# Optimization experiments

Hardware: AMD Instinct MI355X
Metric: run time of the kernel (lower is better)

Reference implementation:

```python
import jax, jax.numpy as jnp
import numpy as np

B, N, H, T = 256, 512, 2048, 64
DT = 0.05  # time spacing so tanh-MLP dynamics stay well-behaved


def setup_inputs() -> dict:
    key = jax.random.key(0)
    k0, k1, k2 = jax.random.split(key, 3)
    y_0 = jax.random.normal(k0, (B, N), dtype=jnp.float32)
    t_eval = jnp.arange(T, dtype=jnp.float32) * DT
    # dy/dt neural network: f(t, y) = tanh(y @ W1 + b1) @ W2 + b2
    W1 = jax.random.normal(k1, (N, H), dtype=jnp.float32) * 0.05
    b1 = jnp.zeros((H,), dtype=jnp.float32)
    W2 = jax.random.normal(k2, (H, N), dtype=jnp.float32) * 0.05
    b2 = jnp.zeros((N,), dtype=jnp.float32)
    return {"y_0": y_0, "t_eval": t_eval, "W1": W1, "b1": b1, "W2": W2, "b2": b2}


def reference(y_0, t_eval, W1, b1, W2, b2):
    """RK4 odeint: returns (y_t [B,T,N], t_t [T], y_loss [B]).

    One classical RK4 step per consecutive pair of t_eval points;
    continuous loss defaults to zero (matches _zero_loss).
    """
    def f(t, y):
        # time-invariant neural dynamics; t kept for signature fidelity
        return jnp.tanh(y @ W1 + b1) @ W2 + b2

    def rk4_step(y, ts):
        t0, t1 = ts[0], ts[1]
        h = t1 - t0
        k1 = f(t0, y)
        k2 = f(t0 + h * 0.5, y + (h * 0.5) * k1)
        k3 = f(t0 + h * 0.5, y + (h * 0.5) * k2)
        k4 = f(t1, y + h * k3)
        y_new = y + (h / 6.0) * (k1 + 2.0 * k2 + 2.0 * k3 + k4)
        return y_new, y_new

    ts_pairs = jnp.stack([t_eval[:-1], t_eval[1:]], axis=1)  # [T-1, 2]
    _, ys = jax.lax.scan(rk4_step, y_0, ts_pairs)            # [T-1, B, N]
    y_t = jnp.concatenate([y_0[None], ys], axis=0)           # [T, B, N]
    y_t = jnpp_transpose(y_t) if False else jnp.transpose(y_t, (1, 0, 2))  # [B, T, N]
    y_loss = jnp.zeros(y_0.shape[:-1], dtype=y_0.dtype)      # zero continuous loss
    return y_t, t_eval, y_loss
```

## Files before the change

kernel.cpp:

```cpp
#include <hip/hip_runtime.h>
#include <hip/hip_bf16.h>

#define Bsz 256
#define Nd  512
#define Hd  2048
#define Td  64
#define OFF_T (Bsz * Td * Nd)
#define OFF_L (OFF_T + Td)
#define LDU 514
#define LDZ 136

typedef __attribute__((ext_vector_type(8))) short short8;
typedef __attribute__((ext_vector_type(4))) float f32x4;

static __device__ __forceinline__ unsigned short f2bf(float x) {
  unsigned u = __builtin_bit_cast(unsigned, x);
  u += 0x7FFFu + ((u >> 16) & 1u);
  return (unsigned short)(u >> 16);
}
static __device__ __forceinline__ float fast_tanh(float x) {
  float ex = __expf(2.0f * x);
  return 1.0f - 2.0f / (ex + 1.0f);
}
static __device__ __forceinline__ unsigned long long lda64(const void* p) {
  return __hip_atomic_load((const unsigned long long*)p, __ATOMIC_RELAXED,
                           __HIP_MEMORY_SCOPE_AGENT);
}
static __device__ __forceinline__ void sta64(void* p, unsigned long long v) {
  __hip_atomic_store((unsigned long long*)p, v, __ATOMIC_RELAXED,
                     __HIP_MEMORY_SCOPE_AGENT);
}
static __device__ __forceinline__ unsigned lda32(const unsigned* p) {
  return __hip_atomic_load(p, __ATOMIC_RELAXED, __HIP_MEMORY_SCOPE_AGENT);
}
static __device__ __forceinline__ void sta32(unsigned* p, unsigned v) {
  __hip_atomic_store(p, v, __ATOMIC_RELAXED, __HIP_MEMORY_SCOPE_AGENT);
}

__launch_bounds__(256, 1)
__global__ void ode_df(const float* __restrict__ y0g, const float* __restrict__ te,
                       const float* __restrict__ W1, const float* __restrict__ b1,
                       const float* __restrict__ W2, const float* __restrict__ b2,
                       float* __restrict__ out, unsigned* __restrict__ flagZ,
                       unsigned* __restrict__ flagK,
                       float* __restrict__ kS, unsigned short* __restrict__ Zg) {
  __shared__ unsigned short Ulds[16 * LDU];
  __shared__ unsigned short Zlds[16 * LDZ];
  __shared__ float red[4][16][33];
  __shared__ char spad[56 * 1024];

  const int blk = blockIdx.x;
  const int g = blk & 15, il = blk >> 4;
  const int tid = threadIdx.x;
  const int wv = tid >> 6, lane = tid & 63;
  const int lr = lane & 15, lk = lane >> 4;

  if (te[0] == 1.0e30f) {
    ((volatile char*)spad)[tid] = (char)tid;
    out[0] = ((volatile char*)spad)[0];
  }

  short8 w1f[2][16];
  {
    const int hbase = il * 128 + wv * 32;
    #pragma unroll
    for (int n = 0; n < 2; ++n) {
      const int col = hbase + n * 16 + lr;
      #pragma unroll
      for (int kt = 0; kt < 16; ++kt) {
        short8 v;
        #pragma unroll
        for (int jj = 0; jj < 8; ++jj)
          v[jj] = (short)f2bf(W1[(kt * 32 + lk * 8 + jj) * Hd + col]);
        w1f[n][kt] = v;
      }
    }
  }
  short8 w2f[2][16];
  {
    #pragma unroll
    for (int n = 0; n < 2; ++n) {
      const int col = il * 32 + n * 16 + lr;
      #pragma unroll
      for (int kt = 0; kt < 16; ++kt) {
        short8 v;
        #pragma unroll
        for (int jj = 0; jj < 8; ++jj)
          v[jj] = (short)f2bf(W2[(wv * 512 + kt * 32 + lk * 8 + jj) * Nd + col]);
        w2f[n][kt] = v;
      }
    }
  }
  float b1c[2];
  b1c[0] = b1[il * 128 + wv * 32 + lr];
  b1c[1] = b1[il * 128 + wv * 32 + 16 + lr];

  const int r  = tid >> 4;
  const int cq = tid & 15;
  const int cb = cq * 32;
  const int rowg = g * 16 + r;
  const int c2 = (tid & 15) * 2;
  const int rowe = tid >> 4;
  const float b2e0 = b2[il * 32 + c2], b2e1 = b2[il * 32 + c2 + 1];

  float yv[32];
  #pragma unroll
  for (int gg = 0; gg < 8; ++gg) {
    f32x4 v = *(const f32x4*)&y0g[rowg * Nd + cb + gg * 4];
    yv[gg * 4 + 0] = v[0]; yv[gg * 4 + 1] = v[1];
    yv[gg * 4 + 2] = v[2]; yv[gg * 4 + 3] = v[3];
  }
  float acc_y[32];
  #pragma unroll
  for (int p = 0; p < 32; ++p) acc_y[p] = 0.0f;

  if (cq == il) {
    #pragma unroll
    for (int gg = 0; gg < 8; ++gg) {
      f32x4 v = {yv[gg * 4], yv[gg * 4 + 1], yv[gg * 4 + 2], yv[gg * 4 + 3]};
      *(f32x4*)&out[rowg * (Td * Nd) + cb + gg * 4] = v;
    }
  }
  if (blk == 0) {
    if (tid < Td) out[OFF_T + tid] = te[tid];
    out[OFF_L + tid] = 0.0f;
  }

  unsigned* flZ = flagZ + g * 16;
  unsigned* flK = flagK + g * 16;

  int j = 0;
  for (int t = 0; t < Td - 1; ++t) {
    const float h = te[t + 1] - te[t];
    for (int e = 1; e <= 4; ++e) {
      float kv[32];
      if (!(e == 1 && t == 0)) {
        const unsigned tgt = (unsigned)j;
        const unsigned* p = flK + (tid & 15);
        for (;;) {
          unsigned v = lda32(p);
          if (__all((int)(v >= tgt))) break;
          __builtin_amdgcn_s_sleep(1);
        }
        const float* kbase = &kS[rowg * Nd + cb];
        #pragma unroll
        for (int p2 = 0; p2 < 16; ++p2) {
          unsigned long long q = lda64(kbase + p2 * 2);
          kv[2 * p2 + 0] = __builtin_bit_cast(float, (unsigned)(q & 0xFFFFFFFFull));
          kv[2 * p2 + 1] = __builtin_bit_cast(float, (unsigned)(q >> 32));
        }
      }
      if (e == 1) {
        if (t > 0) {
          const float hp6 = (te[t] - te[t - 1]) * (1.0f / 6.0f);
          #pragma unroll
          for (int p2 = 0; p2 < 32; ++p2) yv[p2] += hp6 * (acc_y[p2] + kv[p2]);
          if (cq == il) {
            #pragma unroll
            for (int gg = 0; gg < 8; ++gg) {
              f32x4 v = {yv[gg * 4], yv[gg * 4 + 1], yv[gg * 4 + 2], yv[gg * 4 + 3]};
              *(f32x4*)&out[rowg * (Td * Nd) + t * Nd + cb + gg * 4] = v;
            }
          }
        }
        #pragma unroll
        for (int p2 = 0; p2 < 32; ++p2) acc_y[p2] = 0.0f;
        #pragma unroll
        for (int gg = 0; gg < 4; ++gg) {
          short8 s;
          #pragma unroll
          for (int p2 = 0; p2 < 8; ++p2) s[p2] = (short)f2bf(yv[gg * 8 + p2]);
          *(short8*)&Ulds[r * LDU + cb + gg * 8] = s;
        }
      } else {
        const float c = (e == 4) ? h : 0.5f * h;
        const float w = (e == 2) ? 1.0f : 2.0f;
        #pragma unroll
        for (int gg = 0; gg < 4; ++gg) {
          short8 s;
          #pragma unroll
          for (int p2 = 0; p2 < 8; ++p2) {
            const int idx = gg * 8 + p2;
            acc_y[idx] += w * kv[idx];
            s[p2] = (short)f2bf(yv[idx] + c * kv[idx]);
          }
          *(short8*)&Ulds[r * LDU + cb + gg * 8] = s;
        }
      }
      __syncthreads();

      f32x4 acc1_0 = {0.f, 0.f, 0.f, 0.f}, acc1_1 = {0.f, 0.f, 0.f, 0.f};
      {
        const int abase = lr * LDU + lk * 8;
        #pragma unroll
        for (int kt = 0; kt < 16; ++kt) {
          short8 a = *(const short8*)&Ulds[abase + kt * 32];
          acc1_0 = __builtin_amdgcn_mfma_f32_16x16x32_bf16(a, w1f[0][kt], acc1_0, 0, 0, 0);
          acc1_1 = __builtin_amdgcn_mfma_f32_16x16x32_bf16(a, w1f[1][kt], acc1_1, 0, 0, 0);
        }
      }
      #pragma unroll
      for (int n = 0; n < 2; ++n) {
        f32x4 a = n ? acc1_1 : acc1_0;
        #pragma unroll
        for (int q = 0; q < 4; ++q)
          Zlds[(lk * 4 + q) * LDZ + wv * 32 + n * 16 + lr] = f2bf(fast_tanh(a[q] + b1c[n]));
      }
      __syncthreads();
      #pragma unroll
      for (int u = 0; u < 2; ++u) {
        int idx = tid + u * 256;
        int zr = idx >> 5, zc4 = idx & 31;
        unsigned long long v = *(const unsigned long long*)&Zlds[zr * LDZ + zc4 * 4];
        sta64(&Zg[(g * 16 + zr) * Hd + il * 128 + zc4 * 4], v);
      }
      __syncthreads();
      if (tid == 0) sta32(&flZ[il], (unsigned)(j + 1));

      f32x4 acc2_0 = {0.f, 0.f, 0.f, 0.f}, acc2_1 = {0.f, 0.f, 0.f, 0.f};
      {
        const unsigned zt = (unsigned)(j + 1);
        const unsigned short* zp = &Zg[(g * 16 + lr) * Hd + wv * 512 + lk * 8];
        #pragma unroll
        for (int q = 0; q < 4; ++q) {
          const unsigned* fz = &flZ[wv * 4 + q];
          while (lda32(fz) < zt) __builtin_amdgcn_s_sleep(1);
          #pragma unroll
          for (int k2 = 0; k2 < 4; ++k2) {
            const int kt = q * 4 + k2;
            union { unsigned long long q2[2]; short8 s; } az_;
            az_.q2[0] = lda64(zp + kt * 32);
            az_.q2[1] = lda64(zp + kt * 32 + 4);
            acc2_0 = __builtin_amdgcn_mfma_f32_16x16x32_bf16(az_.s, w2f[0][kt], acc2_0, 0, 0, 0);
            acc2_1 = __builtin_amdgcn_mfma_f32_16x16x32_bf16(az_.s, w2f[1][kt], acc2_1, 0, 0, 0);
          }
        }
      }
      #pragma unroll
      for (int q = 0; q < 4; ++q) {
        red[wv][lk * 4 + q][lr]      = acc2_0[q];
        red[wv][lk * 4 + q][16 + lr] = acc2_1[q];
      }
      __syncthreads();
      {
        float s0 = red[0][rowe][c2] + red[1][rowe][c2] + red[2][rowe][c2] + red[3][rowe][c2] + b2e0;
        float s1 = red[0][rowe][c2 + 1] + red[1][rowe][c2 + 1] + red[2][rowe][c2 + 1] + red[3][rowe][c2 + 1] + b2e1;
        unsigned long long pk =
            ((unsigned long long)__builtin_bit_cast(unsigned, s1) << 32) |
            __builtin_bit_cast(unsigned, s0);
        sta64(&kS[(g * 16 + rowe) * Nd + il * 32 + c2], pk);
      }
      __syncthreads();
      if (tid == 0) sta32(&flK[il], (unsigned)(j + 1));
      ++j;
    }
  }

  {
    const unsigned tgt = (unsigned)j;
    const unsigned* p = flK + (tid & 15);
    for (;;) {
      unsigned v = lda32(p);
      if (__all((int)(v >= tgt))) break;
      __builtin_amdgcn_s_sleep(1);
    }
    float kv[32];
    const float* kbase = &kS[rowg * Nd + cb];
    #pragma unroll
    for (int p2 = 0; p2 < 16; ++p2) {
      unsigned long long q = lda64(kbase + p2 * 2);
      kv[2 * p2 + 0] = __builtin_bit_cast(float, (unsigned)(q & 0xFFFFFFFFull));
      kv[2 * p2 + 1] = __builtin_bit_cast(float, (unsigned)(q >> 32));
    }
    const float hp6 = (te[Td - 1] - te[Td - 2]) * (1.0f / 6.0f);
    #pragma unroll
    for (int p2 = 0; p2 < 32; ++p2) yv[p2] += hp6 * (acc_y[p2] + kv[p2]);
    if (cq == il) {
      #pragma unroll
      for (int gg = 0; gg < 8; ++gg) {
        f32x4 v = {yv[gg * 4], yv[gg * 4 + 1], yv[gg * 4 + 2], yv[gg * 4 + 3]};
        *(f32x4*)&out[rowg * (Td * Nd) + (Td - 1) * Nd + cb + gg * 4] = v;
      }
    }
  }
}

extern "C" void kernel_launch(void* const* d_in, const int* in_sizes, int n_in,
                              void* d_out, int out_size, void* d_ws, size_t ws_size,
                              hipStream_t stream) {
  const float* y0 = (const float*)d_in[0];
  const float* te = (const float*)d_in[1];
  const float* W1 = (const float*)d_in[2];
  const float* b1 = (const float*)d_in[3];
  const float* W2 = (const float*)d_in[4];
  const float* b2 = (const float*)d_in[5];
  float* out = (float*)d_out;

  char* p = (char*)d_ws;
  unsigned* flagZ = (unsigned*)p;
  unsigned* flagK = (unsigned*)(p + 1024);
  float* kS = (float*)(p + 4096);
  unsigned short* Zg = (unsigned short*)(p + 4096 + 512 * 1024);

  hipMemsetAsync(d_ws, 0, 4096, stream);
  ode_df<<<dim3(256), dim3(256), 0, stream>>>(y0, te, W1, b1, W2, b2, out,
                                              flagZ, flagK, kS, Zg);
}
```

Baseline: 2.984 ms.

## Replace block-level flags with per-row sequence counters and per-producer data slabs

```diff
diff --git a/kernel.cpp b/kernel.cpp
--- a/kernel.cpp
+++ b/kernel.cpp
@@ -36,14 +36,17 @@
 static __device__ __forceinline__ void sta32(unsigned* p, unsigned v) {
   __hip_atomic_store(p, v, __ATOMIC_RELAXED, __HIP_MEMORY_SCOPE_AGENT);
 }
+static __device__ __forceinline__ void wave_drain() {
+  asm volatile("s_waitcnt vmcnt(0)" ::: "memory");
+}
 
 __launch_bounds__(256, 1)
-__global__ void ode_df(const float* __restrict__ y0g, const float* __restrict__ te,
+__global__ void ode_sq(const float* __restrict__ y0g, const float* __restrict__ te,
                        const float* __restrict__ W1, const float* __restrict__ b1,
                        const float* __restrict__ W2, const float* __restrict__ b2,
-                       float* __restrict__ out, unsigned* __restrict__ flagZ,
-                       unsigned* __restrict__ flagK,
-                       float* __restrict__ kS, unsigned short* __restrict__ Zg) {
+                       float* __restrict__ out, unsigned* __restrict__ seqK,
+                       unsigned* __restrict__ seqZ,
+                       float* __restrict__ kD, unsigned short* __restrict__ ZD) {
   __shared__ unsigned short Ulds[16 * LDU];
   __shared__ unsigned short Zlds[16 * LDZ];
   __shared__ float red[4][16][33];
@@ -103,6 +106,10 @@
   const int rowe = tid >> 4;
   const float b2e0 = b2[il * 32 + c2], b2e1 = b2[il * 32 + c2 + 1];
 
+  const int podbase = g * 16;
+  unsigned* mySeqK = &seqK[(podbase + cq) * 16 + r];
+  const float* myKD = &kD[((podbase + cq) * 16 + r) * 32];
+
   float yv[32];
   #pragma unroll
   for (int gg = 0; gg < 8; ++gg) {
@@ -125,9 +132,6 @@
     if (tid < Td) out[OFF_T + tid] = te[tid];
     out[OFF_L + tid] = 0.0f;
   }
-
-  unsigned* flZ = flagZ + g * 16;
-  unsigned* flK = flagK + g * 16;
 
   int j = 0;
   for (int t = 0; t < Td - 1; ++t) {
@@ -136,16 +140,11 @@
       float kv[32];
       if (!(e == 1 && t == 0)) {
         const unsigned tgt = (unsigned)j;
-        const unsigned* p = flK + (tid & 15);
-        for (;;) {
-          unsigned v = lda32(p);
-          if (__all((int)(v >= tgt))) break;
+        while (!__all((int)(lda32(mySeqK) >= tgt)))
           __builtin_amdgcn_s_sleep(1);
-        }
-        const float* kbase = &kS[rowg * Nd + cb];
         #pragma unroll
         for (int p2 = 0; p2 < 16; ++p2) {
-          unsigned long long q = lda64(kbase + p2 * 2);
+          unsigned long long q = lda64(myKD + p2 * 2);
           kv[2 * p2 + 0] = __builtin_bit_cast(float, (unsigned)(q & 0xFFFFFFFFull));
           kv[2 * p2 + 1] = __builtin_bit_cast(float, (unsigned)(q >> 32));
         }
@@ -207,30 +206,37 @@
           Zlds[(lk * 4 + q) * LDZ + wv * 32 + n * 16 + lr] = f2bf(fast_tanh(a[q] + b1c[n]));
       }
       __syncthreads();
-      #pragma unroll
-      for (int u = 0; u < 2; ++u) {
-        int idx = tid + u * 256;
-        int zr = idx >> 5, zc4 = idx & 31;
-        unsigned long long v = *(const unsigned long long*)&Zlds[zr * LDZ + zc4 * 4];
-        sta64(&Zg[(g * 16 + zr) * Hd + il * 128 + zc4 * 4], v);
-      }
-      __syncthreads();
-      if (tid == 0) sta32(&flZ[il], (unsigned)(j + 1));
+
+      {
+        int zr0 = tid >> 5, zc4 = tid & 31;
+        unsigned long long v0 = *(const unsigned long long*)&Zlds[zr0 * LDZ + zc4 * 4];
+        sta64(&ZD[((podbase + il) * 16 + zr0) * 128 + zc4 * 4], v0);
+        int zr1 = 8 + zr0;
+        unsigned long long v1 = *(const unsigned long long*)&Zlds[zr1 * LDZ + zc4 * 4];
+        sta64(&ZD[((podbase + il) * 16 + zr1) * 128 + zc4 * 4], v1);
+        wave_drain();
+        if ((tid & 31) == 0) {
+          sta32(&seqZ[(podbase + il) * 16 + zr0], (unsigned)(j + 1));
+          sta32(&seqZ[(podbase + il) * 16 + zr1], (unsigned)(j + 1));
+        }
+      }
 
       f32x4 acc2_0 = {0.f, 0.f, 0.f, 0.f}, acc2_1 = {0.f, 0.f, 0.f, 0.f};
       {
         const unsigned zt = (unsigned)(j + 1);
-        const unsigned short* zp = &Zg[(g * 16 + lr) * Hd + wv * 512 + lk * 8];
         #pragma unroll
         for (int q = 0; q < 4; ++q) {
-          const unsigned* fz = &flZ[wv * 4 + q];
-          while (lda32(fz) < zt) __builtin_amdgcn_s_sleep(1);
+          const int m = wv * 4 + q;
+          const unsigned* sp = &seqZ[(podbase + m) * 16 + lr];
+          while (!__all((int)(lda32(sp) >= zt)))
+            __builtin_amdgcn_s_sleep(1);
+          const unsigned short* zp = &ZD[((podbase + m) * 16 + lr) * 128 + lk * 8];
           #pragma unroll
           for (int k2 = 0; k2 < 4; ++k2) {
+            union { unsigned long long q2[2]; short8 s; } az_;
+            az_.q2[0] = lda64(zp + k2 * 32);
+            az_.q2[1] = lda64(zp + k2 * 32 + 4);
             const int kt = q * 4 + k2;
-            union { unsigned long long q2[2]; short8 s; } az_;
-            az_.q2[0] = lda64(zp + kt * 32);
-            az_.q2[1] = lda64(zp + kt * 32 + 4);
             acc2_0 = __builtin_amdgcn_mfma_f32_16x16x32_bf16(az_.s, w2f[0][kt], acc2_0, 0, 0, 0);
             acc2_1 = __builtin_amdgcn_mfma_f32_16x16x32_bf16(az_.s, w2f[1][kt], acc2_1, 0, 0, 0);
           }
@@ -248,27 +254,23 @@
         unsigned long long pk =
             ((unsigned long long)__builtin_bit_cast(unsigned, s1) << 32) |
             __builtin_bit_cast(unsigned, s0);
-        sta64(&kS[(g * 16 + rowe) * Nd + il * 32 + c2], pk);
-      }
-      __syncthreads();
-      if (tid == 0) sta32(&flK[il], (unsigned)(j + 1));
+        sta64(&kD[((podbase + il) * 16 + rowe) * 32 + c2], pk);
+        wave_drain();
+        if ((tid & 15) == 0)
+          sta32(&seqK[(podbase + il) * 16 + rowe], (unsigned)(j + 1));
+      }
       ++j;
     }
   }
 
   {
     const unsigned tgt = (unsigned)j;
-    const unsigned* p = flK + (tid & 15);
-    for (;;) {
-      unsigned v = lda32(p);
-      if (__all((int)(v >= tgt))) break;
+    while (!__all((int)(lda32(mySeqK) >= tgt)))
       __builtin_amdgcn_s_sleep(1);
-    }
     float kv[32];
-    const float* kbase = &kS[rowg * Nd + cb];
     #pragma unroll
     for (int p2 = 0; p2 < 16; ++p2) {
-      unsigned long long q = lda64(kbase + p2 * 2);
+      unsigned long long q = lda64(myKD + p2 * 2);
       kv[2 * p2 + 0] = __builtin_bit_cast(float, (unsigned)(q & 0xFFFFFFFFull));
       kv[2 * p2 + 1] = __builtin_bit_cast(float, (unsigned)(q >> 32));
     }
@@ -297,12 +299,12 @@
   float* out = (float*)d_out;
 
   char* p = (char*)d_ws;
-  unsigned* flagZ = (unsigned*)p;
-  unsigned* flagK = (unsigned*)(p + 1024);
-  float* kS = (float*)(p + 4096);
-  unsigned short* Zg = (unsigned short*)(p + 4096 + 512 * 1024);
-
-  hipMemsetAsync(d_ws, 0, 4096, stream);
-  ode_df<<<dim3(256), dim3(256), 0, stream>>>(y0, te, W1, b1, W2, b2, out,
-                                              flagZ, flagK, kS, Zg);
-}
+  unsigned* seqK = (unsigned*)p;
+  unsigned* seqZ = (unsigned*)(p + 16 * 1024);
+  float* kD = (float*)(p + 32 * 1024);
+  unsigned short* ZD = (unsigned short*)(p + 32 * 1024 + 512 * 1024);
+
+  hipMemsetAsync(d_ws, 0, 32 * 1024, stream);
+  ode_sq<<<dim3(256), dim3(256), 0, stream>>>(y0, te, W1, b1, W2, b2, out,
+                                              seqK, seqZ, kD, ZD);
+}
```

New measurement: 3.699 ms. 24.0% more time.

## Replace flag-based inter-block sync with tagged data words

Applied to the files above, without the earlier changes.

```diff
diff --git a/kernel.cpp b/kernel.cpp
--- a/kernel.cpp
+++ b/kernel.cpp
@@ -12,6 +12,7 @@
 
 typedef __attribute__((ext_vector_type(8))) short short8;
 typedef __attribute__((ext_vector_type(4))) float f32x4;
+typedef __attribute__((ext_vector_type(4))) unsigned u32x4;
 
 static __device__ __forceinline__ unsigned short f2bf(float x) {
   unsigned u = __builtin_bit_cast(unsigned, x);
@@ -30,20 +31,18 @@
   __hip_atomic_store((unsigned long long*)p, v, __ATOMIC_RELAXED,
                      __HIP_MEMORY_SCOPE_AGENT);
 }
-static __device__ __forceinline__ unsigned lda32(const unsigned* p) {
-  return __hip_atomic_load(p, __ATOMIC_RELAXED, __HIP_MEMORY_SCOPE_AGENT);
-}
-static __device__ __forceinline__ void sta32(unsigned* p, unsigned v) {
-  __hip_atomic_store(p, v, __ATOMIC_RELAXED, __HIP_MEMORY_SCOPE_AGENT);
+static __device__ __forceinline__ unsigned long long tagf32(float x, unsigned tag) {
+  return (unsigned long long)__builtin_bit_cast(unsigned, x) |
+         ((unsigned long long)tag << 32);
 }
 
 __launch_bounds__(256, 1)
-__global__ void ode_df(const float* __restrict__ y0g, const float* __restrict__ te,
+__global__ void ode_tg(const float* __restrict__ y0g, const float* __restrict__ te,
                        const float* __restrict__ W1, const float* __restrict__ b1,
                        const float* __restrict__ W2, const float* __restrict__ b2,
-                       float* __restrict__ out, unsigned* __restrict__ flagZ,
-                       unsigned* __restrict__ flagK,
-                       float* __restrict__ kS, unsigned short* __restrict__ Zg) {
+                       float* __restrict__ out,
+                       unsigned long long* __restrict__ kD,
+                       unsigned long long* __restrict__ ZD) {
   __shared__ unsigned short Ulds[16 * LDU];
   __shared__ unsigned short Zlds[16 * LDZ];
   __shared__ float red[4][16][33];
@@ -103,6 +102,8 @@
   const int rowe = tid >> 4;
   const float b2e0 = b2[il * 32 + c2], b2e1 = b2[il * 32 + c2 + 1];
 
+  unsigned long long* myK = &kD[((size_t)g * 16 + r) * 512 + cb];
+
   float yv[32];
   #pragma unroll
   for (int gg = 0; gg < 8; ++gg) {
@@ -125,9 +126,6 @@
     if (tid < Td) out[OFF_T + tid] = te[tid];
     out[OFF_L + tid] = 0.0f;
   }
-
-  unsigned* flZ = flagZ + g * 16;
-  unsigned* flK = flagK + g * 16;
 
   int j = 0;
   for (int t = 0; t < Td - 1; ++t) {
@@ -136,19 +134,19 @@
       float kv[32];
       if (!(e == 1 && t == 0)) {
         const unsigned tgt = (unsigned)j;
-        const unsigned* p = flK + (tid & 15);
+        unsigned long long w[32];
         for (;;) {
-          unsigned v = lda32(p);
-          if (__all((int)(v >= tgt))) break;
+          #pragma unroll
+          for (int i = 0; i < 32; ++i) w[i] = lda64(myK + i);
+          bool ok = true;
+          #pragma unroll
+          for (int i = 0; i < 32; ++i) ok &= ((unsigned)(w[i] >> 32) == tgt);
+          if (__all((int)ok)) break;
           __builtin_amdgcn_s_sleep(1);
         }
-        const float* kbase = &kS[rowg * Nd + cb];
-        #pragma unroll
-        for (int p2 = 0; p2 < 16; ++p2) {
-          unsigned long long q = lda64(kbase + p2 * 2);
-          kv[2 * p2 + 0] = __builtin_bit_cast(float, (unsigned)(q & 0xFFFFFFFFull));
-          kv[2 * p2 + 1] = __builtin_bit_cast(float, (unsigned)(q >> 32));
-        }
+        #pragma unroll
+        for (int i = 0; i < 32; ++i)
+          kv[i] = __builtin_bit_cast(float, (unsigned)w[i]);
       }
       if (e == 1) {
         if (t > 0) {
@@ -207,32 +205,48 @@
           Zlds[(lk * 4 + q) * LDZ + wv * 32 + n * 16 + lr] = f2bf(fast_tanh(a[q] + b1c[n]));
       }
       __syncthreads();
-      #pragma unroll
-      for (int u = 0; u < 2; ++u) {
-        int idx = tid + u * 256;
-        int zr = idx >> 5, zc4 = idx & 31;
-        unsigned long long v = *(const unsigned long long*)&Zlds[zr * LDZ + zc4 * 4];
-        sta64(&Zg[(g * 16 + zr) * Hd + il * 128 + zc4 * 4], v);
-      }
-      __syncthreads();
-      if (tid == 0) sta32(&flZ[il], (unsigned)(j + 1));
+
+      {
+        const unsigned long long tz = (unsigned long long)(unsigned)(j + 1) << 32;
+        unsigned long long* zb = &ZD[(((size_t)g * 16 + il) * 16) * 64];
+        #pragma unroll
+        for (int u = 0; u < 4; ++u) {
+          int W = tid + u * 256;
+          int zrow = W >> 6, cp = W & 63;
+          unsigned zpair = *(const unsigned*)&Zlds[zrow * LDZ + cp * 2];
+          sta64(zb + zrow * 64 + cp, (unsigned long long)zpair | tz);
+        }
+      }
 
       f32x4 acc2_0 = {0.f, 0.f, 0.f, 0.f}, acc2_1 = {0.f, 0.f, 0.f, 0.f};
       {
         const unsigned zt = (unsigned)(j + 1);
-        const unsigned short* zp = &Zg[(g * 16 + lr) * Hd + wv * 512 + lk * 8];
         #pragma unroll
         for (int q = 0; q < 4; ++q) {
-          const unsigned* fz = &flZ[wv * 4 + q];
-          while (lda32(fz) < zt) __builtin_amdgcn_s_sleep(1);
+          const int m = wv * 4 + q;
+          const unsigned long long* zw =
+              &ZD[(((size_t)g * 16 + m) * 16 + lr) * 64 + lk * 4];
+          unsigned long long w[16];
+          for (;;) {
+            #pragma unroll
+            for (int k2 = 0; k2 < 4; ++k2)
+              #pragma unroll
+              for (int i = 0; i < 4; ++i)
+                w[k2 * 4 + i] = lda64(zw + k2 * 16 + i);
+            bool ok = true;
+            #pragma unroll
+            for (int i = 0; i < 16; ++i) ok &= ((unsigned)(w[i] >> 32) == zt);
+            if (__all((int)ok)) break;
+            __builtin_amdgcn_s_sleep(1);
+          }
           #pragma unroll
           for (int k2 = 0; k2 < 4; ++k2) {
+            u32x4 pw = {(unsigned)w[k2 * 4 + 0], (unsigned)w[k2 * 4 + 1],
+                        (unsigned)w[k2 * 4 + 2], (unsigned)w[k2 * 4 + 3]};
+            short8 az = __builtin_bit_cast(short8, pw);
             const int kt = q * 4 + k2;
-            union { unsigned long long q2[2]; short8 s; } az_;
-            az_.q2[0] = lda64(zp + kt * 32);
-            az_.q2[1] = lda64(zp + kt * 32 + 4);
-            acc2_0 = __builtin_amdgcn_mfma_f32_16x16x32_bf16(az_.s, w2f[0][kt], acc2_0, 0, 0, 0);
-            acc2_1 = __builtin_amdgcn_mfma_f32_16x16x32_bf16(az_.s, w2f[1][kt], acc2_1, 0, 0, 0);
+            acc2_0 = __builtin_amdgcn_mfma_f32_16x16x32_bf16(az, w2f[0][kt], acc2_0, 0, 0, 0);
+            acc2_1 = __builtin_amdgcn_mfma_f32_16x16x32_bf16(az, w2f[1][kt], acc2_1, 0, 0, 0);
           }
         }
       }
@@ -245,36 +259,31 @@
       {
         float s0 = red[0][rowe][c2] + red[1][rowe][c2] + red[2][rowe][c2] + red[3][rowe][c2] + b2e0;
         float s1 = red[0][rowe][c2 + 1] + red[1][rowe][c2 + 1] + red[2][rowe][c2 + 1] + red[3][rowe][c2 + 1] + b2e1;
-        unsigned long long pk =
-            ((unsigned long long)__builtin_bit_cast(unsigned, s1) << 32) |
-            __builtin_bit_cast(unsigned, s0);
-        sta64(&kS[(g * 16 + rowe) * Nd + il * 32 + c2], pk);
-      }
-      __syncthreads();
-      if (tid == 0) sta32(&flK[il], (unsigned)(j + 1));
+        const unsigned tk = (unsigned)(j + 1);
+        unsigned long long* kb = &kD[((size_t)g * 16 + rowe) * 512 + il * 32 + c2];
+        sta64(kb,     tagf32(s0, tk));
+        sta64(kb + 1, tagf32(s1, tk));
+      }
       ++j;
     }
   }
 
   {
     const unsigned tgt = (unsigned)j;
-    const unsigned* p = flK + (tid & 15);
+    unsigned long long w[32];
     for (;;) {
-      unsigned v = lda32(p);
-      if (__all((int)(v >= tgt))) break;
+      #pragma unroll
+      for (int i = 0; i < 32; ++i) w[i] = lda64(myK + i);
+      bool ok = true;
+      #pragma unroll
+      for (int i = 0; i < 32; ++i) ok &= ((unsigned)(w[i] >> 32) == tgt);
+      if (__all((int)ok)) break;
       __builtin_amdgcn_s_sleep(1);
-    }
-    float kv[32];
-    const float* kbase = &kS[rowg * Nd + cb];
-    #pragma unroll
-    for (int p2 = 0; p2 < 16; ++p2) {
-      unsigned long long q = lda64(kbase + p2 * 2);
-      kv[2 * p2 + 0] = __builtin_bit_cast(float, (unsigned)(q & 0xFFFFFFFFull));
-      kv[2 * p2 + 1] = __builtin_bit_cast(float, (unsigned)(q >> 32));
     }
     const float hp6 = (te[Td - 1] - te[Td - 2]) * (1.0f / 6.0f);
     #pragma unroll
-    for (int p2 = 0; p2 < 32; ++p2) yv[p2] += hp6 * (acc_y[p2] + kv[p2]);
+    for (int p2 = 0; p2 < 32; ++p2)
+      yv[p2] += hp6 * (acc_y[p2] + __builtin_bit_cast(float, (unsigned)w[p2]));
     if (cq == il) {
       #pragma unroll
       for (int gg = 0; gg < 8; ++gg) {
@@ -297,12 +306,9 @@
   float* out = (float*)d_out;
 
   char* p = (char*)d_ws;
-  unsigned* flagZ = (unsigned*)p;
-  unsigned* flagK = (unsigned*)(p + 1024);
-  float* kS = (float*)(p + 4096);
-  unsigned short* Zg = (unsigned short*)(p + 4096 + 512 * 1024);
-
-  hipMemsetAsync(d_ws, 0, 4096, stream);
-  ode_df<<<dim3(256), dim3(256), 0, stream>>>(y0, te, W1, b1, W2, b2, out,
-                                              flagZ, flagK, kS, Zg);
-}
+  unsigned long long* kD = (unsigned long long*)p;
+  unsigned long long* ZD = (unsigned long long*)(p + (1 << 20));
+
+  hipMemsetAsync(d_ws, 0, 3 << 20, stream);
+  ode_tg<<<dim3(256), dim3(256), 0, stream>>>(y0, te, W1, b1, W2, b2, out, kD, ZD);
+}
```

Measured after the change: 5.777 ms. 93.6% more time.

## Split batch into two interleaved halves to overlap cross-block sync with compute

Applied to the files above, without the earlier changes.

```diff
diff --git a/kernel.cpp b/kernel.cpp
--- a/kernel.cpp
+++ b/kernel.cpp
@@ -8,7 +8,7 @@
 #define OFF_T (Bsz * Td * Nd)
 #define OFF_L (OFF_T + Td)
 #define LDU 514
-#define LDZ 136
+#define LDZ 68
 
 typedef __attribute__((ext_vector_type(8))) short short8;
 typedef __attribute__((ext_vector_type(4))) float f32x4;
@@ -36,21 +36,26 @@
 static __device__ __forceinline__ void sta32(unsigned* p, unsigned v) {
   __hip_atomic_store(p, v, __ATOMIC_RELAXED, __HIP_MEMORY_SCOPE_AGENT);
 }
+static __device__ __forceinline__ void pollf(const unsigned* f, unsigned tgt) {
+  const unsigned* p = f + (threadIdx.x & 31);
+  while (!__all((int)(lda32(p) >= tgt)))
+    __builtin_amdgcn_s_sleep(1);
+}
 
 __launch_bounds__(256, 1)
-__global__ void ode_df(const float* __restrict__ y0g, const float* __restrict__ te,
+__global__ void ode_pl(const float* __restrict__ y0g, const float* __restrict__ te,
                        const float* __restrict__ W1, const float* __restrict__ b1,
                        const float* __restrict__ W2, const float* __restrict__ b2,
                        float* __restrict__ out, unsigned* __restrict__ flagZ,
                        unsigned* __restrict__ flagK,
-                       float* __restrict__ kS, unsigned short* __restrict__ Zg) {
+                       float* __restrict__ kX, unsigned short* __restrict__ ZX) {
   __shared__ unsigned short Ulds[16 * LDU];
   __shared__ unsigned short Zlds[16 * LDZ];
-  __shared__ float red[4][16][33];
-  __shared__ char spad[56 * 1024];
+  __shared__ float red[2][4][16][17];
+  __shared__ char spad[54 * 1024];
 
   const int blk = blockIdx.x;
-  const int g = blk & 15, il = blk >> 4;
+  const int g = blk & 7, il = blk >> 3;
   const int tid = threadIdx.x;
   const int wv = tid >> 6, lane = tid & 63;
   const int lr = lane & 15, lk = lane >> 4;
@@ -60,65 +65,57 @@
     out[0] = ((volatile char*)spad)[0];
   }
 
-  short8 w1f[2][16];
+  short8 w1f[16];
   {
-    const int hbase = il * 128 + wv * 32;
-    #pragma unroll
-    for (int n = 0; n < 2; ++n) {
-      const int col = hbase + n * 16 + lr;
+    const int col = il * 64 + wv * 16 + lr;
+    #pragma unroll
+    for (int kt = 0; kt < 16; ++kt) {
+      short8 v;
       #pragma unroll
-      for (int kt = 0; kt < 16; ++kt) {
-        short8 v;
-        #pragma unroll
-        for (int jj = 0; jj < 8; ++jj)
-          v[jj] = (short)f2bf(W1[(kt * 32 + lk * 8 + jj) * Hd + col]);
-        w1f[n][kt] = v;
-      }
-    }
-  }
-  short8 w2f[2][16];
+      for (int jj = 0; jj < 8; ++jj)
+        v[jj] = (short)f2bf(W1[(kt * 32 + lk * 8 + jj) * Hd + col]);
+      w1f[kt] = v;
+    }
+  }
+  short8 w2f[16];
   {
-    #pragma unroll
-    for (int n = 0; n < 2; ++n) {
-      const int col = il * 32 + n * 16 + lr;
+    const int col = il * 16 + lr;
+    #pragma unroll
+    for (int kt = 0; kt < 16; ++kt) {
+      short8 v;
       #pragma unroll
-      for (int kt = 0; kt < 16; ++kt) {
-        short8 v;
-        #pragma unroll
-        for (int jj = 0; jj < 8; ++jj)
-          v[jj] = (short)f2bf(W2[(wv * 512 + kt * 32 + lk * 8 + jj) * Nd + col]);
-        w2f[n][kt] = v;
-      }
-    }
-  }
-  float b1c[2];
-  b1c[0] = b1[il * 128 + wv * 32 + lr];
-  b1c[1] = b1[il * 128 + wv * 32 + 16 + lr];
+      for (int jj = 0; jj < 8; ++jj)
+        v[jj] = (short)f2bf(W2[(wv * 512 + kt * 32 + lk * 8 + jj) * Nd + col]);
+      w2f[kt] = v;
+    }
+  }
+  const float b1c = b1[il * 64 + wv * 16 + lr];
+  const float b2e = b2[il * 16 + (tid & 15)];
 
   const int r  = tid >> 4;
   const int cq = tid & 15;
   const int cb = cq * 32;
-  const int rowg = g * 16 + r;
-  const int c2 = (tid & 15) * 2;
-  const int rowe = tid >> 4;
-  const float b2e0 = b2[il * 32 + c2], b2e1 = b2[il * 32 + c2 + 1];
-
-  float yv[32];
+  const int rowA = g * 32 + r;
+  const int rowB = g * 32 + 16 + r;
+
+  float yvA[32], yvB[32], accA[32], accB[32];
   #pragma unroll
   for (int gg = 0; gg < 8; ++gg) {
-    f32x4 v = *(const f32x4*)&y0g[rowg * Nd + cb + gg * 4];
-    yv[gg * 4 + 0] = v[0]; yv[gg * 4 + 1] = v[1];
-    yv[gg * 4 + 2] = v[2]; yv[gg * 4 + 3] = v[3];
-  }
-  float acc_y[32];
+    f32x4 va = *(const f32x4*)&y0g[rowA * Nd + cb + gg * 4];
+    f32x4 vb = *(const f32x4*)&y0g[rowB * Nd + cb + gg * 4];
+    #pragma unroll
+    for (int q = 0; q < 4; ++q) { yvA[gg * 4 + q] = va[q]; yvB[gg * 4 + q] = vb[q]; }
+  }
   #pragma unroll
-  for (int p = 0; p < 32; ++p) acc_y[p] = 0.0f;
-
-  if (cq == il) {
+  for (int p = 0; p < 32; ++p) { accA[p] = 0.0f; accB[p] = 0.0f; }
+
+  if (il == cq) {
     #pragma unroll
     for (int gg = 0; gg < 8; ++gg) {
-      f32x4 v = {yv[gg * 4], yv[gg * 4 + 1], yv[gg * 4 + 2], yv[gg * 4 + 3]};
-      *(f32x4*)&out[rowg * (Td * Nd) + cb + gg * 4] = v;
+      f32x4 va = {yvA[gg * 4], yvA[gg * 4 + 1], yvA[gg * 4 + 2], yvA[gg * 4 + 3]};
+      *(f32x4*)&out[rowA * (Td * Nd) + cb + gg * 4] = va;
+      f32x4 vb = {yvB[gg * 4], yvB[gg * 4 + 1], yvB[gg * 4 + 2], yvB[gg * 4 + 3]};
+      *(f32x4*)&out[rowB * (Td * Nd) + cb + gg * 4] = vb;
     }
   }
   if (blk == 0) {
@@ -126,160 +123,157 @@
     out[OFF_L + tid] = 0.0f;
   }
 
-  unsigned* flZ = flagZ + g * 16;
-  unsigned* flK = flagK + g * 16;
+  unsigned* fZA = flagZ + g * 32;
+  unsigned* fZB = flagZ + (8 + g) * 32;
+  unsigned* fKA = flagK + g * 32;
+  unsigned* fKB = flagK + (8 + g) * 32;
+  float* kXA = kX;
+  float* kXB = kX + (size_t)8 * 16 * 512;
+  unsigned short* ZXA = ZX;
+  unsigned short* ZXB = ZX + (size_t)8 * 32 * 16 * 64;
+  const float* myKA = kXA + ((size_t)g * 16 + r) * 512 + cb;
+  const float* myKB = kXB + ((size_t)g * 16 + r) * 512 + cb;
+
+#define LOADKV(KV, SRC)                                                      \
+  { _Pragma("unroll")                                                        \
+    for (int p2 = 0; p2 < 16; ++p2) {                                        \
+      unsigned long long q_ = lda64((SRC) + p2 * 2);                         \
+      KV[2 * p2]     = __builtin_bit_cast(float, (unsigned)(q_ & 0xFFFFFFFFull)); \
+      KV[2 * p2 + 1] = __builtin_bit_cast(float, (unsigned)(q_ >> 32));      \
+    } }
+
+#define UPHASE(YV, ACC, ROWG, KV)                                            \
+  do {                                                                       \
+    if (e == 1) {                                                            \
+      if (t > 0) {                                                           \
+        const float hp6_ = (te[t] - te[t - 1]) * (1.0f / 6.0f);              \
+        _Pragma("unroll")                                                    \
+        for (int p2 = 0; p2 < 32; ++p2) YV[p2] += hp6_ * (ACC[p2] + KV[p2]); \
+        if (il == cq) {                                                      \
+          _Pragma("unroll")                                                  \
+          for (int gg = 0; gg < 8; ++gg) {                                   \
+            f32x4 v_ = {YV[gg*4], YV[gg*4+1], YV[gg*4+2], YV[gg*4+3]};       \
+            *(f32x4*)&out[(ROWG) * (Td * Nd) + t * Nd + cb + gg * 4] = v_;   \
+          }                                                                  \
+        }                                                                    \
+      }                                                                      \
+      _Pragma("unroll")                                                      \
+      for (int p2 = 0; p2 < 32; ++p2) ACC[p2] = 0.0f;                        \
+      _Pragma("unroll")                                                      \
+      for (int gg = 0; gg < 4; ++gg) {                                       \
+        short8 s_;                                                           \
+        _Pragma("unroll")                                                    \
+        for (int p2 = 0; p2 < 8; ++p2) s_[p2] = (short)f2bf(YV[gg * 8 + p2]);\
+        *(short8*)&Ulds[r * LDU + cb + gg * 8] = s_;                         \
+      }                                                                      \
+    } else {                                                                 \
+      const float cc_ = (e == 4) ? h : 0.5f * h;                             \
+      const float ww_ = (e == 2) ? 1.0f : 2.0f;                              \
+      _Pragma("unroll")                                                      \
+      for (int gg = 0; gg < 4; ++gg) {                                       \
+        short8 s_;                                                           \
+        _Pragma("unroll")                                                    \
+        for (int p2 = 0; p2 < 8; ++p2) {                                     \
+          const int idx_ = gg * 8 + p2;                                      \
+          ACC[idx_] += ww_ * KV[idx_];                                       \
+          s_[p2] = (short)f2bf(YV[idx_] + cc_ * KV[idx_]);                   \
+        }                                                                    \
+        *(short8*)&Ulds[r * LDU + cb + gg * 8] = s_;                         \
+      }                                                                      \
+    }                                                                        \
+  } while (0)
+
+#define GEMM1()                                                              \
+  { f32x4 a1_ = {0.f, 0.f, 0.f, 0.f};                                        \
+    const int abase_ = lr * LDU + lk * 8;                                    \
+    _Pragma("unroll")                                                        \
+    for (int kt = 0; kt < 16; ++kt) {                                        \
+      short8 a_ = *(const short8*)&Ulds[abase_ + kt * 32];                   \
+      a1_ = __builtin_amdgcn_mfma_f32_16x16x32_bf16(a_, w1f[kt], a1_, 0,0,0);\
+    }                                                                        \
+    _Pragma("unroll")                                                        \
+    for (int q = 0; q < 4; ++q)                                              \
+      Zlds[(lk * 4 + q) * LDZ + wv * 16 + lr] = f2bf(fast_tanh(a1_[q] + b1c)); }
+
+#define EXPORTZ(ZC)                                                          \
+  { unsigned long long v_ =                                                  \
+        *(const unsigned long long*)&Zlds[(tid >> 4) * LDZ + (tid & 15) * 4];\
+    sta64(&(ZC)[((size_t)(g * 32 + il) * 16 + (tid >> 4)) * 64 + (tid & 15) * 4], v_); }
+
+#define GEMM2(ZC, RC)                                                        \
+  { f32x4 a2_ = {0.f, 0.f, 0.f, 0.f};                                        \
+    _Pragma("unroll")                                                        \
+    for (int kt = 0; kt < 16; ++kt) {                                        \
+      const int m_ = wv * 8 + (kt >> 1);                                     \
+      const unsigned short* zp_ =                                            \
+          (ZC) + ((size_t)(g * 32 + m_) * 16 + lr) * 64 + (kt & 1) * 32 + lk * 8; \
+      union { unsigned long long q2[2]; short8 s; } az_;                     \
+      az_.q2[0] = lda64(zp_); az_.q2[1] = lda64(zp_ + 4);                    \
+      a2_ = __builtin_amdgcn_mfma_f32_16x16x32_bf16(az_.s, w2f[kt], a2_, 0,0,0); \
+    }                                                                        \
+    _Pragma("unroll")                                                        \
+    for (int q = 0; q < 4; ++q) red[RC][wv][lk * 4 + q][lr] = a2_[q]; }
+
+#define SUMEXPK(RC, KC)                                                      \
+  { const int kr_ = tid >> 4, kc_ = tid & 15;                                \
+    float s_ = red[RC][0][kr_][kc_] + red[RC][1][kr_][kc_]                   \
+             + red[RC][2][kr_][kc_] + red[RC][3][kr_][kc_] + b2e;            \
+    sta32((unsigned*)&(KC)[((size_t)g * 16 + kr_) * 512 + il * 16 + kc_],    \
+          __builtin_bit_cast(unsigned, s_)); }
 
   int j = 0;
   for (int t = 0; t < Td - 1; ++t) {
     const float h = te[t + 1] - te[t];
     for (int e = 1; e <= 4; ++e) {
       float kv[32];
-      if (!(e == 1 && t == 0)) {
-        const unsigned tgt = (unsigned)j;
-        const unsigned* p = flK + (tid & 15);
-        for (;;) {
-          unsigned v = lda32(p);
-          if (__all((int)(v >= tgt))) break;
-          __builtin_amdgcn_s_sleep(1);
-        }
-        const float* kbase = &kS[rowg * Nd + cb];
-        #pragma unroll
-        for (int p2 = 0; p2 < 16; ++p2) {
-          unsigned long long q = lda64(kbase + p2 * 2);
-          kv[2 * p2 + 0] = __builtin_bit_cast(float, (unsigned)(q & 0xFFFFFFFFull));
-          kv[2 * p2 + 1] = __builtin_bit_cast(float, (unsigned)(q >> 32));
-        }
-      }
-      if (e == 1) {
-        if (t > 0) {
-          const float hp6 = (te[t] - te[t - 1]) * (1.0f / 6.0f);
-          #pragma unroll
-          for (int p2 = 0; p2 < 32; ++p2) yv[p2] += hp6 * (acc_y[p2] + kv[p2]);
-          if (cq == il) {
-            #pragma unroll
-            for (int gg = 0; gg < 8; ++gg) {
-              f32x4 v = {yv[gg * 4], yv[gg * 4 + 1], yv[gg * 4 + 2], yv[gg * 4 + 3]};
-              *(f32x4*)&out[rowg * (Td * Nd) + t * Nd + cb + gg * 4] = v;
-            }
-          }
-        }
-        #pragma unroll
-        for (int p2 = 0; p2 < 32; ++p2) acc_y[p2] = 0.0f;
-        #pragma unroll
-        for (int gg = 0; gg < 4; ++gg) {
-          short8 s;
-          #pragma unroll
-          for (int p2 = 0; p2 < 8; ++p2) s[p2] = (short)f2bf(yv[gg * 8 + p2]);
-          *(short8*)&Ulds[r * LDU + cb + gg * 8] = s;
-        }
-      } else {
-        const float c = (e == 4) ? h : 0.5f * h;
-        const float w = (e == 2) ? 1.0f : 2.0f;
-        #pragma unroll
-        for (int gg = 0; gg < 4; ++gg) {
-          short8 s;
-          #pragma unroll
-          for (int p2 = 0; p2 < 8; ++p2) {
-            const int idx = gg * 8 + p2;
-            acc_y[idx] += w * kv[idx];
-            s[p2] = (short)f2bf(yv[idx] + c * kv[idx]);
-          }
-          *(short8*)&Ulds[r * LDU + cb + gg * 8] = s;
-        }
-      }
-      __syncthreads();
-
-      f32x4 acc1_0 = {0.f, 0.f, 0.f, 0.f}, acc1_1 = {0.f, 0.f, 0.f, 0.f};
-      {
-        const int abase = lr * LDU + lk * 8;
-        #pragma unroll
-        for (int kt = 0; kt < 16; ++kt) {
-          short8 a = *(const short8*)&Ulds[abase + kt * 32];
-          acc1_0 = __builtin_amdgcn_mfma_f32_16x16x32_bf16(a, w1f[0][kt], acc1_0, 0, 0, 0);
-          acc1_1 = __builtin_amdgcn_mfma_f32_16x16x32_bf16(a, w1f[1][kt], acc1_1, 0, 0, 0);
-        }
-      }
-      #pragma unroll
-      for (int n = 0; n < 2; ++n) {
-        f32x4 a = n ? acc1_1 : acc1_0;
-        #pragma unroll
-        for (int q = 0; q < 4; ++q)
-          Zlds[(lk * 4 + q) * LDZ + wv * 32 + n * 16 + lr] = f2bf(fast_tanh(a[q] + b1c[n]));
-      }
-      __syncthreads();
-      #pragma unroll
-      for (int u = 0; u < 2; ++u) {
-        int idx = tid + u * 256;
-        int zr = idx >> 5, zc4 = idx & 31;
-        unsigned long long v = *(const unsigned long long*)&Zlds[zr * LDZ + zc4 * 4];
-        sta64(&Zg[(g * 16 + zr) * Hd + il * 128 + zc4 * 4], v);
-      }
-      __syncthreads();
-      if (tid == 0) sta32(&flZ[il], (unsigned)(j + 1));
-
-      f32x4 acc2_0 = {0.f, 0.f, 0.f, 0.f}, acc2_1 = {0.f, 0.f, 0.f, 0.f};
-      {
-        const unsigned zt = (unsigned)(j + 1);
-        const unsigned short* zp = &Zg[(g * 16 + lr) * Hd + wv * 512 + lk * 8];
-        #pragma unroll
-        for (int q = 0; q < 4; ++q) {
-          const unsigned* fz = &flZ[wv * 4 + q];
-          while (lda32(fz) < zt) __builtin_amdgcn_s_sleep(1);
-          #pragma unroll
-          for (int k2 = 0; k2 < 4; ++k2) {
-            const int kt = q * 4 + k2;
-            union { unsigned long long q2[2]; short8 s; } az_;
-            az_.q2[0] = lda64(zp + kt * 32);
-            az_.q2[1] = lda64(zp + kt * 32 + 4);
-            acc2_0 = __builtin_amdgcn_mfma_f32_16x16x32_bf16(az_.s, w2f[0][kt], acc2_0, 0, 0, 0);
-            acc2_1 = __builtin_amdgcn_mfma_f32_16x16x32_bf16(az_.s, w2f[1][kt], acc2_1, 0, 0, 0);
-          }
-        }
-      }
-      #pragma unroll
-      for (int q = 0; q < 4; ++q) {
-        red[wv][lk * 4 + q][lr]      = acc2_0[q];
-        red[wv][lk * 4 + q][16 + lr] = acc2_1[q];
-      }
-      __syncthreads();
-      {
-        float s0 = red[0][rowe][c2] + red[1][rowe][c2] + red[2][rowe][c2] + red[3][rowe][c2] + b2e0;
-        float s1 = red[0][rowe][c2 + 1] + red[1][rowe][c2 + 1] + red[2][rowe][c2 + 1] + red[3][rowe][c2 + 1] + b2e1;
-        unsigned long long pk =
-            ((unsigned long long)__builtin_bit_cast(unsigned, s1) << 32) |
-            __builtin_bit_cast(unsigned, s0);
-        sta64(&kS[(g * 16 + rowe) * Nd + il * 32 + c2], pk);
-      }
-      __syncthreads();
-      if (tid == 0) sta32(&flK[il], (unsigned)(j + 1));
+      if (!(e == 1 && t == 0)) { pollf(fKA, (unsigned)j); LOADKV(kv, myKA); }
+      UPHASE(yvA, accA, rowA, kv);
+      __syncthreads();
+      if (tid == 0 && j > 0) sta32(&fKB[il], (unsigned)j);
+      GEMM1();
+      __syncthreads();
+      EXPORTZ(ZXA);
+      if (!(e == 1 && t == 0)) { pollf(fKB, (unsigned)j); LOADKV(kv, myKB); }
+      UPHASE(yvB, accB, rowB, kv);
+      __syncthreads();
+      if (tid == 0) sta32(&fZA[il], (unsigned)(j + 1));
+      GEMM1();
+      __syncthreads();
+      EXPORTZ(ZXB);
+      pollf(fZA, (unsigned)(j + 1));
+      GEMM2(ZXA, 0);
+      __syncthreads();
+      if (tid == 0) sta32(&fZB[il], (unsigned)(j + 1));
+      SUMEXPK(0, kXA);
+      pollf(fZB, (unsigned)(j + 1));
+      GEMM2(ZXB, 1);
+      __syncthreads();
+      if (tid == 0) sta32(&fKA[il], (unsigned)(j + 1));
+      SUMEXPK(1, kXB);
       ++j;
     }
   }
 
+  __syncthreads();
+  if (tid == 0) sta32(&fKB[il], (unsigned)j);
   {
-    const unsigned tgt = (unsigned)j;
-    const unsigned* p = flK + (tid & 15);
-    for (;;) {
-      unsigned v = lda32(p);
-      if (__all((int)(v >= tgt))) break;
-      __builtin_amdgcn_s_sleep(1);
-    }
+    const float hp6 = (te[Td - 1] - te[Td - 2]) * (1.0f / 6.0f);
     float kv[32];
-    const float* kbase = &kS[rowg * Nd + cb];
-    #pragma unroll
-    for (int p2 = 0; p2 < 16; ++p2) {
-      unsigned long long q = lda64(kbase + p2 * 2);
-      kv[2 * p2 + 0] = __builtin_bit_cast(float, (unsigned)(q & 0xFFFFFFFFull));
-      kv[2 * p2 + 1] = __builtin_bit_cast(float, (unsigned)(q >> 32));
-    }
-    const float hp6 = (te[Td - 1] - te[Td - 2]) * (1.0f / 6.0f);
-    #pragma unroll
-    for (int p2 = 0; p2 < 32; ++p2) yv[p2] += hp6 * (acc_y[p2] + kv[p2]);
-    if (cq == il) {
+    pollf(fKA, (unsigned)j);
+    LOADKV(kv, myKA);
+    #pragma unroll
+    for (int p2 = 0; p2 < 32; ++p2) yvA[p2] += hp6 * (accA[p2] + kv[p2]);
+    pollf(fKB, (unsigned)j);
+    LOADKV(kv, myKB);
+    #pragma unroll
+    for (int p2 = 0; p2 < 32; ++p2) yvB[p2] += hp6 * (accB[p2] + kv[p2]);
+    if (il == cq) {
       #pragma unroll
       for (int gg = 0; gg < 8; ++gg) {
-        f32x4 v = {yv[gg * 4], yv[gg * 4 + 1], yv[gg * 4 + 2], yv[gg * 4 + 3]};
-        *(f32x4*)&out[rowg * (Td * Nd) + (Td - 1) * Nd + cb + gg * 4] = v;
+        f32x4 va = {yvA[gg * 4], yvA[gg * 4 + 1], yvA[gg * 4 + 2], yvA[gg * 4 + 3]};
+        *(f32x4*)&out[rowA * (Td * Nd) + (Td - 1) * Nd + cb + gg * 4] = va;
+        f32x4 vb = {yvB[gg * 4], yvB[gg * 4 + 1], yvB[gg * 4 + 2], yvB[gg * 4 + 3]};
+        *(f32x4*)&out[rowB * (Td * Nd) + (Td - 1) * Nd + cb + gg * 4] = vb;
       }
     }
   }
@@ -298,11 +292,11 @@
 
   char* p = (char*)d_ws;
   unsigned* flagZ = (unsigned*)p;
-  unsigned* flagK = (unsigned*)(p + 1024);
-  float* kS = (float*)(p + 4096);
-  unsigned short* Zg = (unsigned short*)(p + 4096 + 512 * 1024);
+  unsigned* flagK = (unsigned*)(p + 2048);
+  float* kX = (float*)(p + 4096);
+  unsigned short* ZX = (unsigned short*)(p + 4096 + 512 * 1024);
 
   hipMemsetAsync(d_ws, 0, 4096, stream);
-  ode_df<<<dim3(256), dim3(256), 0, stream>>>(y0, te, W1, b1, W2, b2, out,
-                                              flagZ, flagK, kS, Zg);
-}
+  ode_pl<<<dim3(256), dim3(256), 0, stream>>>(y0, te, W1, b1, W2, b2, out,
+                                              flagZ, flagK, kX, ZX);
+}
```

New measurement: 5.301 ms. 1.78x slower.
